# Kernel tuning notes

Hardware: AMD Instinct MI355X
Metric: run time of the kernel (lower is better)

## Reference

```python
import jax, jax.numpy as jnp
import numpy as np

INPUT_DIM = 1024
OUTPUT_DIM = 1024
SPLINE_POINTS = 4

def setup_inputs() -> dict:
    key = jax.random.key(0)
    k1, k2 = jax.random.split(key)
    x = jax.random.normal(k1, (4096, INPUT_DIM), dtype=jnp.float32)
    spline_coeffs = jax.random.normal(k2, (OUTPUT_DIM, INPUT_DIM, SPLINE_POINTS, 4), dtype=jnp.float32)
    return {"x": x, "spline_coeffs": spline_coeffs}

def reference(x, spline_coeffs):
    # Per-feature min-max normalization over the batch dim (as in the torch code,
    # where x[:, j].min()/max() are taken over the batch).
    xmin = jnp.min(x, axis=0, keepdims=True)   # [1, D]
    xmax = jnp.max(x, axis=0, keepdims=True)
    xn = (x - xmin) / (xmax - xmin)            # [B, D]

    # The original sums the cubic polynomial over all spline_points, so the
    # effective coefficients are the sum over the spline_points axis.
    c = jnp.sum(spline_coeffs, axis=2)         # [O, D, 4]

    x2 = xn * xn
    x3 = x2 * xn
    # out[b, o] = sum_d c0*x^3 + c1*x^2 + c2*x + c3
    out = (jnp.einsum('bd,od->bo', x3, c[..., 0])
           + jnp.einsum('bd,od->bo', x2, c[..., 1])
           + jnp.einsum('bd,od->bo', xn, c[..., 2])
           + jnp.sum(c[..., 3], axis=1)[None, :])
    return out
```

## Files before the change

kernel.cpp:

```cpp
#include <hip/hip_runtime.h>
#include <hip/hip_bf16.h>
#include <stdint.h>
#include <stddef.h>

typedef __bf16 bf16;
typedef __attribute__((ext_vector_type(4))) __bf16 bf16x4;
typedef __attribute__((ext_vector_type(8))) __bf16 bf16x8;
typedef __attribute__((ext_vector_type(4))) float f32x4;

#define BATCH 4096
#define DIM 1024
#define ODIM 1024
#define K3 3072

#define WS_P      0
#define WS_CB     25165824
#define WS_BIAS   31457280
#define WS_PMIN   31461376
#define WS_PMAX   31723520
#define WS_MINV   31985664
#define WS_SCALE  31989760

#define ASYNC16(g, l)                                                          \
  __builtin_amdgcn_global_load_lds(                                            \
      (__attribute__((address_space(1))) void*)(g),                            \
      (__attribute__((address_space(3))) void*)(l), 16, 0, 0)

#define WAIT_VM(n) __builtin_amdgcn_s_waitcnt(0x0F00 | 0x0070 | ((n)&15) | ((((n)>>4)&3)<<14))
#define BARRIER()                     \
  do {                                \
    asm volatile("" ::: "memory");    \
    __builtin_amdgcn_s_barrier();     \
    asm volatile("" ::: "memory");    \
  } while (0)

__global__ void k_minmax_part(const float* __restrict__ x,
                              float* __restrict__ pmin,
                              float* __restrict__ pmax) {
  const int t = threadIdx.x;
  const int ch = blockIdx.x;
  const float* p = x + (size_t)ch * 64 * DIM + (t << 2);
  f32x4 mn = {1e30f, 1e30f, 1e30f, 1e30f};
  f32x4 mx = {-1e30f, -1e30f, -1e30f, -1e30f};
#pragma unroll 8
  for (int r = 0; r < 64; ++r) {
    f32x4 v = *(const f32x4*)(p + (size_t)r * DIM);
#pragma unroll
    for (int j = 0; j < 4; ++j) {
      mn[j] = fminf(mn[j], v[j]);
      mx[j] = fmaxf(mx[j], v[j]);
    }
  }
  *(f32x4*)(pmin + ch * DIM + (t << 2)) = mn;
  *(f32x4*)(pmax + ch * DIM + (t << 2)) = mx;
}

__global__ void k_minmax_final(const float* __restrict__ pmin,
                               const float* __restrict__ pmax,
                               float* __restrict__ minv,
                               float* __restrict__ scale) {
  int col = blockIdx.x * 256 + threadIdx.x;
  float mn = 1e30f, mx = -1e30f;
#pragma unroll 8
  for (int ch = 0; ch < 64; ++ch) {
    mn = fminf(mn, pmin[ch * DIM + col]);
    mx = fmaxf(mx, pmax[ch * DIM + col]);
  }
  minv[col] = mn;
  scale[col] = 1.0f / (mx - mn);
}

__global__ void k_prep(const float* __restrict__ x,
                       const float* __restrict__ minv,
                       const float* __restrict__ scale,
                       bf16* __restrict__ P,
                       const float* __restrict__ sp,
                       bf16* __restrict__ CB,
                       float* __restrict__ bias) {
  __shared__ float red[4];
  const int t = threadIdx.x;
  if (blockIdx.x < BATCH) {
    const int b = blockIdx.x;
    const int d = t << 2;
    f32x4 xv = *(const f32x4*)(x + (size_t)b * DIM + d);
    f32x4 mn = *(const f32x4*)(minv + d);
    f32x4 sc = *(const f32x4*)(scale + d);
    bf16x4 o3, o2, o1;
#pragma unroll
    for (int j = 0; j < 4; ++j) {
      float xn = (xv[j] - mn[j]) * sc[j];
      float x2 = xn * xn;
      float x3 = x2 * xn;
      o3[j] = (bf16)x3;
      o2[j] = (bf16)x2;
      o1[j] = (bf16)xn;
    }
    size_t base = (size_t)b * K3 + d;
    *(bf16x4*)(P + base) = o3;
    *(bf16x4*)(P + base + 1024) = o2;
    *(bf16x4*)(P + base + 2048) = o1;
  } else {
    const int o = blockIdx.x - BATCH;
    const int d = t << 2;
    f32x4 s[4];
#pragma unroll
    for (int dd = 0; dd < 4; ++dd) {
      const float* p = sp + ((size_t)o * DIM + d + dd) * 16;
      f32x4 acc = *(const f32x4*)(p);
      acc += *(const f32x4*)(p + 4);
      acc += *(const f32x4*)(p + 8);
      acc += *(const f32x4*)(p + 12);
      s[dd] = acc;
    }
    size_t cb = (size_t)o * K3 + d;
    bf16x4 c0 = {(bf16)s[0][0], (bf16)s[1][0], (bf16)s[2][0], (bf16)s[3][0]};
    bf16x4 c1 = {(bf16)s[0][1], (bf16)s[1][1], (bf16)s[2][1], (bf16)s[3][1]};
    bf16x4 c2 = {(bf16)s[0][2], (bf16)s[1][2], (bf16)s[2][2], (bf16)s[3][2]};
    *(bf16x4*)(CB + cb) = c0;
    *(bf16x4*)(CB + cb + 1024) = c1;
    *(bf16x4*)(CB + cb + 2048) = c2;
    float v = s[0][3] + s[1][3] + s[2][3] + s[3][3];
#pragma unroll
    for (int off = 32; off > 0; off >>= 1) v += __shfl_down(v, off, 64);
    int lane = t & 63, w = t >> 6;
    if (lane == 0) red[w] = v;
    __syncthreads();
    if (t == 0) bias[o] = red[0] + red[1] + red[2] + red[3];
  }
}

#define BM 128
#define BN 128
#define BKE 64
#define NIT (K3 / BKE)
__global__ __launch_bounds__(256, 1) void k_gemm(const bf16* __restrict__ P,
                                                 const bf16* __restrict__ CBm,
                                                 const float* __restrict__ bias,
                                                 float* __restrict__ out) {
  __shared__ bf16 ldsm[2][2][BM * BKE];

  const int tid = threadIdx.x;
  const int wave = tid >> 6;
  const int lane = tid & 63;
  const int bm = blockIdx.x * BM;
  const int bn = blockIdx.y * BN;
  const int wr = (wave >> 1) * 64;
  const int wc = (wave & 1) * 64;

  const size_t rowbytes = (size_t)K3 * 2;

  const char* gAp[4];
  const char* gBp[4];
  int ldso[4];
#pragma unroll
  for (int i = 0; i < 4; ++i) {
    int off = i * 4096 + tid * 16;
    int row = off >> 7;
    int q = (off >> 4) & 7;
    int gb = (q ^ (row & 7)) * 16;
    gAp[i] = (const char*)P + (size_t)(bm + row) * rowbytes + gb;
    gBp[i] = (const char*)CBm + (size_t)(bn + row) * rowbytes + gb;
    ldso[i] = i * 4096 + wave * 1024;
  }

  f32x4 acc[4][4] = {};

  const int mrow = lane & 15;
  const int kq = lane >> 4;

#define STAGE(buf, kt)                                                        \
  do {                                                                        \
    const size_t kb_ = (size_t)(kt) * (BKE * 2);                              \
    char* lA_ = (char*)&ldsm[buf][0][0];                                      \
    char* lB_ = (char*)&ldsm[buf][1][0];                                      \
    _Pragma("unroll") for (int i_ = 0; i_ < 4; ++i_)                          \
        ASYNC16(gAp[i_] + kb_, lA_ + ldso[i_]);                               \
    _Pragma("unroll") for (int i_ = 0; i_ < 4; ++i_)                          \
        ASYNC16(gBp[i_] + kb_, lB_ + ldso[i_]);                               \
  } while (0)

#define COMPUTE(buf)                                                          \
  do {                                                                        \
    const bf16* sA_ = &ldsm[buf][0][0];                                       \
    const bf16* sB_ = &ldsm[buf][1][0];                                       \
    _Pragma("unroll") for (int ks = 0; ks < 2; ++ks) {                        \
      bf16x8 af[4], bg[4];                                                    \
      _Pragma("unroll") for (int i = 0; i < 4; ++i) {                         \
        int row = wr + i * 16 + mrow;                                         \
        int sq = (ks * 4 + kq) ^ (row & 7);                                   \
        af[i] = *(const bf16x8*)&sA_[row * BKE + sq * 8];                     \
      }                                                                       \
      _Pragma("unroll") for (int j = 0; j < 4; ++j) {                         \
        int row = wc + j * 16 + mrow;                                         \
        int sq = (ks * 4 + kq) ^ (row & 7);                                   \
        bg[j] = *(const bf16x8*)&sB_[row * BKE + sq * 8];                     \
      }                                                                       \
      _Pragma("unroll") for (int i = 0; i < 4; ++i)                           \
          _Pragma("unroll") for (int j = 0; j < 4; ++j)                       \
              acc[i][j] = __builtin_amdgcn_mfma_f32_16x16x32_bf16(            \
                  af[i], bg[j], acc[i][j], 0, 0, 0);                          \
    }                                                                         \
  } while (0)

  STAGE(0, 0);
#pragma unroll 2
  for (int kt = 0; kt < NIT - 1; ++kt) {
    const int cur = kt & 1;
    STAGE(cur ^ 1, kt + 1);
    WAIT_VM(8);
    BARRIER();
    COMPUTE(cur);
    BARRIER();
  }
  WAIT_VM(0);
  BARRIER();
  COMPUTE((NIT - 1) & 1);

  const int ccol = lane & 15;
  const int crow = (lane >> 4) * 4;
#pragma unroll
  for (int j = 0; j < 4; ++j) {
    const int col = bn + wc + j * 16 + ccol;
    const float bv = bias[col];
#pragma unroll
    for (int i = 0; i < 4; ++i) {
      const int row0 = bm + wr + i * 16 + crow;
#pragma unroll
      for (int r = 0; r < 4; ++r)
        out[(size_t)(row0 + r) * ODIM + col] = acc[i][j][r] + bv;
    }
  }
#undef STAGE
#undef COMPUTE
}

extern "C" void kernel_launch(void* const* d_in, const int* in_sizes, int n_in,
                              void* d_out, int out_size, void* d_ws, size_t ws_size,
                              hipStream_t stream) {
  (void)in_sizes; (void)n_in; (void)out_size; (void)ws_size;
  const float* x = (const float*)d_in[0];
  const float* sp = (const float*)d_in[1];
  float* out = (float*)d_out;
  char* ws = (char*)d_ws;

  bf16* Pm = (bf16*)(ws + WS_P);
  bf16* CBm = (bf16*)(ws + WS_CB);
  float* bias = (float*)(ws + WS_BIAS);
  float* pmin = (float*)(ws + WS_PMIN);
  float* pmax = (float*)(ws + WS_PMAX);
  float* minv = (float*)(ws + WS_MINV);
  float* scale = (float*)(ws + WS_SCALE);

  k_minmax_part<<<64, 256, 0, stream>>>(x, pmin, pmax);
  k_minmax_final<<<4, 256, 0, stream>>>(pmin, pmax, minv, scale);
  k_prep<<<BATCH + ODIM, 256, 0, stream>>>(x, minv, scale, Pm, sp, CBm, bias);
  k_gemm<<<dim3(BATCH / BM, ODIM / BN), 256, 0, stream>>>(Pm, CBm, bias, out);
}
```

Before: 164.9 us.

## Deepen GEMM LDS pipeline to four stages and widen prep/minmax parallelism

The GEMM moves from double buffering to a four-buffer LDS ring with three tiles prefetched ahead, plus an explicit drain of the last three tiles. This is meant to hide global-load latency better. The min/max partial reduction now uses 256 chunks of 16 rows instead of 64 chunks of 64, so more blocks run in parallel. The prep kernel handles 8 features per thread with 16-byte bf16 stores. LDS use grows to 128KB per block, and the final min/max pass reads more partials.

```diff
diff --git a/kernel.cpp b/kernel.cpp
--- a/kernel.cpp
+++ b/kernel.cpp
@@ -17,9 +17,9 @@
 #define WS_CB     25165824
 #define WS_BIAS   31457280
 #define WS_PMIN   31461376
-#define WS_PMAX   31723520
-#define WS_MINV   31985664
-#define WS_SCALE  31989760
+#define WS_PMAX   32509952
+#define WS_MINV   33558528
+#define WS_SCALE  33562624
 
 #define ASYNC16(g, l)                                                          \
   __builtin_amdgcn_global_load_lds(                                            \
@@ -39,11 +39,11 @@
                               float* __restrict__ pmax) {
   const int t = threadIdx.x;
   const int ch = blockIdx.x;
-  const float* p = x + (size_t)ch * 64 * DIM + (t << 2);
+  const float* p = x + (size_t)ch * 16 * DIM + (t << 2);
   f32x4 mn = {1e30f, 1e30f, 1e30f, 1e30f};
   f32x4 mx = {-1e30f, -1e30f, -1e30f, -1e30f};
-#pragma unroll 8
-  for (int r = 0; r < 64; ++r) {
+#pragma unroll
+  for (int r = 0; r < 16; ++r) {
     f32x4 v = *(const f32x4*)(p + (size_t)r * DIM);
 #pragma unroll
     for (int j = 0; j < 4; ++j) {
@@ -62,7 +62,7 @@
   int col = blockIdx.x * 256 + threadIdx.x;
   float mn = 1e30f, mx = -1e30f;
 #pragma unroll 8
-  for (int ch = 0; ch < 64; ++ch) {
+  for (int ch = 0; ch < 256; ++ch) {
     mn = fminf(mn, pmin[ch * DIM + col]);
     mx = fmaxf(mx, pmax[ch * DIM + col]);
   }
@@ -79,28 +79,37 @@
                        float* __restrict__ bias) {
   __shared__ float red[4];
   const int t = threadIdx.x;
-  if (blockIdx.x < BATCH) {
-    const int b = blockIdx.x;
-    const int d = t << 2;
-    f32x4 xv = *(const f32x4*)(x + (size_t)b * DIM + d);
-    f32x4 mn = *(const f32x4*)(minv + d);
-    f32x4 sc = *(const f32x4*)(scale + d);
-    bf16x4 o3, o2, o1;
+  if (blockIdx.x < (BATCH / 2)) {
+    const int b = blockIdx.x * 2 + (t >> 7);
+    const int d = (t & 127) << 3;
+    f32x4 xv0 = *(const f32x4*)(x + (size_t)b * DIM + d);
+    f32x4 xv1 = *(const f32x4*)(x + (size_t)b * DIM + d + 4);
+    f32x4 mn0 = *(const f32x4*)(minv + d);
+    f32x4 mn1 = *(const f32x4*)(minv + d + 4);
+    f32x4 sc0 = *(const f32x4*)(scale + d);
+    f32x4 sc1 = *(const f32x4*)(scale + d + 4);
+    bf16x8 o3, o2, o1;
 #pragma unroll
     for (int j = 0; j < 4; ++j) {
-      float xn = (xv[j] - mn[j]) * sc[j];
+      float xn = (xv0[j] - mn0[j]) * sc0[j];
       float x2 = xn * xn;
       float x3 = x2 * xn;
       o3[j] = (bf16)x3;
       o2[j] = (bf16)x2;
       o1[j] = (bf16)xn;
+      float yn = (xv1[j] - mn1[j]) * sc1[j];
+      float y2 = yn * yn;
+      float y3 = y2 * yn;
+      o3[j + 4] = (bf16)y3;
+      o2[j + 4] = (bf16)y2;
+      o1[j + 4] = (bf16)yn;
     }
     size_t base = (size_t)b * K3 + d;
-    *(bf16x4*)(P + base) = o3;
-    *(bf16x4*)(P + base + 1024) = o2;
-    *(bf16x4*)(P + base + 2048) = o1;
+    *(bf16x8*)(P + base) = o3;
+    *(bf16x8*)(P + base + 1024) = o2;
+    *(bf16x8*)(P + base + 2048) = o1;
   } else {
-    const int o = blockIdx.x - BATCH;
+    const int o = blockIdx.x - (BATCH / 2);
     const int d = t << 2;
     f32x4 s[4];
 #pragma unroll
@@ -133,11 +142,12 @@
 #define BN 128
 #define BKE 64
 #define NIT (K3 / BKE)
+#define NBUF 4
 __global__ __launch_bounds__(256, 1) void k_gemm(const bf16* __restrict__ P,
                                                  const bf16* __restrict__ CBm,
                                                  const float* __restrict__ bias,
                                                  float* __restrict__ out) {
-  __shared__ bf16 ldsm[2][2][BM * BKE];
+  __shared__ bf16 ldsm[NBUF][2][BM * BKE];
 
   const int tid = threadIdx.x;
   const int wave = tid >> 6;
@@ -203,18 +213,27 @@
   } while (0)
 
   STAGE(0, 0);
-#pragma unroll 2
-  for (int kt = 0; kt < NIT - 1; ++kt) {
-    const int cur = kt & 1;
-    STAGE(cur ^ 1, kt + 1);
-    WAIT_VM(8);
+  STAGE(1, 1);
+  STAGE(2, 2);
+#pragma unroll 4
+  for (int kt = 0; kt < NIT - 3; ++kt) {
+    STAGE((kt + 3) & 3, kt + 3);
+    WAIT_VM(24);
     BARRIER();
-    COMPUTE(cur);
+    COMPUTE(kt & 3);
     BARRIER();
   }
+  WAIT_VM(16);
+  BARRIER();
+  COMPUTE(1);
+  BARRIER();
+  WAIT_VM(8);
+  BARRIER();
+  COMPUTE(2);
+  BARRIER();
   WAIT_VM(0);
   BARRIER();
-  COMPUTE((NIT - 1) & 1);
+  COMPUTE(3);
 
   const int ccol = lane & 15;
   const int crow = (lane >> 4) * 4;
@@ -251,8 +270,8 @@
   float* minv = (float*)(ws + WS_MINV);
   float* scale = (float*)(ws + WS_SCALE);
 
-  k_minmax_part<<<64, 256, 0, stream>>>(x, pmin, pmax);
+  k_minmax_part<<<256, 256, 0, stream>>>(x, pmin, pmax);
   k_minmax_final<<<4, 256, 0, stream>>>(pmin, pmax, minv, scale);
-  k_prep<<<BATCH + ODIM, 256, 0, stream>>>(x, minv, scale, Pm, sp, CBm, bias);
+  k_prep<<<(BATCH / 2) + ODIM, 256, 0, stream>>>(x, minv, scale, Pm, sp, CBm, bias);
   k_gemm<<<dim3(BATCH / BM, ODIM / BN), 256, 0, stream>>>(Pm, CBm, bias, out);
 }
```

New measurement: 168.2 us. Within noise of the previous version (+2.0%).
